# Optimization experiments

Measured on AMD Instinct MI355X. Metric: run time of the kernel, lower is better.

## Reference

```python
import jax, jax.numpy as jnp
import numpy as np

N = 50000
E = 800000
D_IN = 256
HID = 256
EPS = 1e-12


def _glorot(key, shape):
    fan_in, fan_out = shape[1], shape[0]
    lim = jnp.sqrt(6.0 / (fan_in + fan_out))
    return jax.random.uniform(key, shape, jnp.float32, -lim, lim)


def setup_inputs() -> dict:
    key = jax.random.key(0)
    ks = jax.random.split(key, 8)
    x = jax.random.normal(ks[0], (N, D_IN), jnp.float32)
    edge_index = jax.random.randint(ks[1], (2, E), 0, N, jnp.int64)
    # SAGEConv params: lin_l (neighbor, with bias), lin_r (root, no bias)
    W1l = _glorot(ks[2], (HID, D_IN))
    b1l = jnp.zeros((HID,), jnp.float32)
    W1r = _glorot(ks[3], (HID, D_IN))
    W2l = _glorot(ks[4], (HID, HID))
    b2l = jnp.zeros((HID,), jnp.float32)
    W2r = _glorot(ks[5], (HID, HID))
    return {"x": x, "edge_index": edge_index,
            "W1l": W1l, "b1l": b1l, "W1r": W1r,
            "W2l": W2l, "b2l": b2l, "W2r": W2r}


def _sage_conv(x, src, dst, Wl, bl, Wr, num_nodes):
    # mean aggregation of source features onto destination nodes
    agg = jax.ops.segment_sum(x[src], dst, num_segments=num_nodes)          # [N, d]
    cnt = jax.ops.segment_sum(jnp.ones((src.shape[0],), x.dtype), dst,
                              num_segments=num_nodes)                        # [N]
    mean = agg / jnp.maximum(cnt, 1.0)[:, None]
    out = mean @ Wl.T + bl + x @ Wr.T                                        # [N, out]
    # L2 normalize (normalize=True)
    norm = jnp.linalg.norm(out, axis=-1, keepdims=True)
    return out / jnp.maximum(norm, EPS)


def reference(x, edge_index, W1l, b1l, W1r, W2l, b2l, W2r):
    src, dst = edge_index[0], edge_index[1]
    n = x.shape[0]
    h = _sage_conv(x, src, dst, W1l, b1l, W1r, n)
    h = jax.nn.relu(h)
    h = _sage_conv(h, src, dst, W2l, b2l, W2r, n)
    return h
```

## Files before the change

kernel.cpp:

```cpp
#include <hip/hip_runtime.h>
#include <hip/hip_bf16.h>


#define DD 256
#define NPB 128

typedef unsigned short ushort_t;
using bf16x8 = __attribute__((ext_vector_type(8))) short;
using f32x4  = __attribute__((ext_vector_type(4))) float;

static __device__ __forceinline__ float b2f(ushort_t u) {
    __hip_bfloat16 h = *reinterpret_cast<__hip_bfloat16*>(&u);
    return __bfloat162float(h);
}
static __device__ __forceinline__ ushort_t f2b(float f) {
    __hip_bfloat16 h = __float2bfloat16(f);
    return *reinterpret_cast<ushort_t*>(&h);
}

static __device__ __forceinline__ void load16(const ushort_t* g, ushort_t* l) {
    __builtin_amdgcn_global_load_lds(
        (const __attribute__((address_space(1))) unsigned*)(g),
        (__attribute__((address_space(3))) unsigned*)(l),
        16, 0, 0);
}


__global__ __launch_bounds__(256) void prep_kernel(
        const int* __restrict__ ei, int* __restrict__ cnt, int E, int eb,
        const float* __restrict__ x, ushort_t* __restrict__ abuf, int xe, int cxb,
        const float* __restrict__ w1l, const float* __restrict__ w1r,
        const float* __restrict__ w2l, const float* __restrict__ w2r,
        ushort_t* __restrict__ wc1, ushort_t* __restrict__ wc2) {
    int b = blockIdx.x;
    if (b < eb) {
        int e = b * 256 + threadIdx.x;
        if (e < E) atomicAdd(&cnt[ei[E + e]], 1);
        return;
    }
    b -= eb;
    if (b < cxb) {
        int i = (b * 256 + threadIdx.x) * 8;
        if (i + 8 > xe) return;
        int row = i >> 8, col = i & 255;
        float4 a = *(const float4*)(x + i);
        float4 c = *(const float4*)(x + i + 4);
        ushort_t o[8] = {f2b(a.x), f2b(a.y), f2b(a.z), f2b(a.w),
                         f2b(c.x), f2b(c.y), f2b(c.z), f2b(c.w)};
        *(int4*)(abuf + (size_t)row * 512 + 256 + col) = *(const int4*)o;
        return;
    }
    b -= cxb;
    {
        int i = (b * 256 + threadIdx.x) * 8;
        int which = i >> 16;
        int o = i & 65535;
        int row = o >> 8, col = o & 255;
        const float* src = (which == 0) ? w1l : (which == 1) ? w1r
                          : (which == 2) ? w2l : w2r;
        ushort_t* dst = ((which < 2) ? wc1 : wc2)
                        + (size_t)row * 512 + (which & 1) * 256 + col;
        float4 a = *(const float4*)(src + o);
        float4 c = *(const float4*)(src + o + 4);
        ushort_t ov[8] = {f2b(a.x), f2b(a.y), f2b(a.z), f2b(a.w),
                          f2b(c.x), f2b(c.y), f2b(c.z), f2b(c.w)};
        *(int4*)dst = *(const int4*)ov;
    }
}


__global__ __launch_bounds__(256) void scan_partial_kernel(const int* __restrict__ cnt,
                                                           int* __restrict__ part, int n) {
    __shared__ int ws[4];
    int tid = threadIdx.x;
    int wave = tid >> 6, lane = tid & 63;
    int i0 = blockIdx.x * 2048 + tid * 8;
    int sum = 0;
    if (i0 + 8 <= n) {
        int4 a = *(const int4*)(cnt + i0);
        int4 b = *(const int4*)(cnt + i0 + 4);
        sum = a.x + a.y + a.z + a.w + b.x + b.y + b.z + b.w;
    } else {
        for (int j = i0; j < n; j++) sum += cnt[j];
    }
    #pragma unroll
    for (int off = 1; off < 64; off <<= 1) sum += __shfl_xor(sum, off);
    if (lane == 0) ws[wave] = sum;
    __syncthreads();
    if (tid == 0) part[blockIdx.x] = ws[0] + ws[1] + ws[2] + ws[3];
}

__global__ __launch_bounds__(256) void scan_final_kernel(const int* __restrict__ cnt,
                                                         const int* __restrict__ part,
                                                         int* __restrict__ offs,
                                                         int* __restrict__ bcur,
                                                         int n, int E, int nb) {
    __shared__ int wt[4];
    __shared__ int sbase;
    int tid = threadIdx.x;
    int wave = tid >> 6, lane = tid & 63;
    if (tid < 64) {
        int pv = (tid < nb) ? part[tid] : 0;
        int incl = pv;
        #pragma unroll
        for (int off = 1; off < 64; off <<= 1) {
            int t = __shfl_up(incl, off);
            if (tid >= off) incl += t;
        }
        if (tid == (int)blockIdx.x) sbase = incl - pv;
    }
    int i0 = blockIdx.x * 2048 + tid * 8;
    int v[8], s[8];
    int run = 0;
    if (i0 + 8 <= n) {
        int4 a = *(const int4*)(cnt + i0);
        int4 b = *(const int4*)(cnt + i0 + 4);
        v[0] = a.x; v[1] = a.y; v[2] = a.z; v[3] = a.w;
        v[4] = b.x; v[5] = b.y; v[6] = b.z; v[7] = b.w;
    } else {
        #pragma unroll
        for (int j = 0; j < 8; j++) v[j] = (i0 + j < n) ? cnt[i0 + j] : 0;
    }
    #pragma unroll
    for (int j = 0; j < 8; j++) { run += v[j]; s[j] = run; }
    int tsum = run;
    int incl = tsum;
    #pragma unroll
    for (int off = 1; off < 64; off <<= 1) {
        int t = __shfl_up(incl, off);
        if (lane >= off) incl += t;
    }
    if (lane == 63) wt[wave] = incl;
    __syncthreads();
    int woff = 0;
    for (int w = 0; w < wave; w++) woff += wt[w];
    int texcl = sbase + woff + (incl - tsum);
    #pragma unroll
    for (int j = 0; j < 8; j++) {
        int idx = i0 + j;
        if (idx < n) {
            int e = texcl + s[j] - v[j];
            offs[idx] = e;
            if ((idx & (NPB - 1)) == 0) bcur[idx / NPB] = e;
        }
    }
    if (blockIdx.x == 0 && tid == 0) offs[n] = E;
}


__global__ __launch_bounds__(256) void part_kernel(const int* __restrict__ ei,
                                                   int* __restrict__ bcur,
                                                   int2* __restrict__ stage,
                                                   int E, int nbuck) {
    __shared__ int hist[512];
    __shared__ int gbase[512];
    int tid = threadIdx.x;
    for (int i = tid; i < nbuck; i += 256) hist[i] = 0;
    __syncthreads();
    int sv[8], dv[8], bk[8], rk[8];
    #pragma unroll
    for (int j = 0; j < 8; j++) {
        int e = blockIdx.x * 2048 + j * 256 + tid;
        if (e < E) {
            sv[j] = ei[e];
            dv[j] = ei[E + e];
            bk[j] = dv[j] / NPB;
            rk[j] = atomicAdd(&hist[bk[j]], 1);
        } else bk[j] = -1;
    }
    __syncthreads();
    for (int i = tid; i < nbuck; i += 256) {
        int h = hist[i];
        gbase[i] = h ? atomicAdd(&bcur[i], h) : 0;
    }
    __syncthreads();
    #pragma unroll
    for (int j = 0; j < 8; j++)
        if (bk[j] >= 0) {
            int p = gbase[bk[j]] + rk[j];
            stage[p] = make_int2(sv[j], dv[j]);
        }
}

__global__ __launch_bounds__(256) void group_kernel(const int2* __restrict__ stage,
                                                    const int* __restrict__ offs,
                                                    int* __restrict__ csr, int N) {
    __shared__ int lcur[NPB];
    int b = blockIdx.x;
    int lo = b * NPB;
    int hi = min(N, lo + NPB);
    int tid = threadIdx.x;
    if (tid < hi - lo) lcur[tid] = offs[lo + tid];
    __syncthreads();
    int base = offs[lo];
    int m = offs[hi] - base;
    for (int t = tid; t < m; t += 256) {
        int2 v = stage[base + t];
        int p = atomicAdd(&lcur[v.y - lo], 1);
        csr[p] = v.x;
    }
}


static __device__ __forceinline__ void add8(float* acc, int4 v) {
    const unsigned* u = (const unsigned*)&v;
    #pragma unroll
    for (int j = 0; j < 4; j++) {
        acc[2 * j]     += __uint_as_float(u[j] << 16);
        acc[2 * j + 1] += __uint_as_float(u[j] & 0xffff0000u);
    }
}

__global__ __launch_bounds__(256) void agg_kernel(const ushort_t* __restrict__ X,
                                                  const int* __restrict__ csr,
                                                  const int* __restrict__ offs,
                                                  ushort_t* __restrict__ mean, int N) {
    int wv = threadIdx.x >> 6;
    int lane = threadIdx.x & 63;
    int half = lane >> 5;
    int c = lane & 31;
    int node = blockIdx.x * 4 + wv;
    if (node >= N) return;
    int beg = offs[node], end = offs[node + 1];

    float acc[8];
    #pragma unroll
    for (int j = 0; j < 8; j++) acc[j] = 0.f;

    const ushort_t* base = X + (size_t)c * 8;
    int i = beg;
    for (; i + 8 <= end; i += 8) {
        int s0 = csr[i + half];
        int s1 = csr[i + 2 + half];
        int s2 = csr[i + 4 + half];
        int s3 = csr[i + 6 + half];
        int4 v0 = *(const int4*)(base + (size_t)s0 * 512);
        int4 v1 = *(const int4*)(base + (size_t)s1 * 512);
        int4 v2 = *(const int4*)(base + (size_t)s2 * 512);
        int4 v3 = *(const int4*)(base + (size_t)s3 * 512);
        add8(acc, v0); add8(acc, v1); add8(acc, v2); add8(acc, v3);
    }
    for (; i + 2 <= end; i += 2) {
        int s0 = csr[i + half];
        int4 v0 = *(const int4*)(base + (size_t)s0 * 512);
        add8(acc, v0);
    }
    if (i < end && half == 0) {
        int s0 = csr[i];
        int4 v0 = *(const int4*)(base + (size_t)s0 * 512);
        add8(acc, v0);
    }

    #pragma unroll
    for (int j = 0; j < 8; j++) acc[j] += __shfl_xor(acc[j], 32);

    if (half == 0) {
        float scale = 1.f / fmaxf((float)(end - beg), 1.f);
        ushort_t o[8];
        #pragma unroll
        for (int j = 0; j < 8; j++) o[j] = f2b(acc[j] * scale);
        *(int4*)(mean + (size_t)node * 512 + c * 8) = *(const int4*)o;
    }
}


__global__ __launch_bounds__(512, 4) void gemm_norm_kernel(
        const ushort_t* __restrict__ abuf,
        const ushort_t* __restrict__ W,
        const float*    __restrict__ bias,
        ushort_t* __restrict__ outb,
        float*    __restrict__ outf,
        int ostride,
        int N, int relu) {
    __shared__ union {
        struct {
            ushort_t As[128 * 64];
            ushort_t Bs[256 * 64];
        } s;
        ushort_t ebuf[64 * 264];
    } u;
    __shared__ float rowsq[128];

    int tid = threadIdx.x;
    int wave = tid >> 6, lane = tid & 63;
    int quad = lane >> 4, m16 = lane & 15;
    int swz = m16 & 7;
    int rowhalf = wave >> 2;
    int colq = wave & 3;
    int rowbase = blockIdx.x * 128;

    if (tid < 128) rowsq[tid] = 0.f;

    f32x4 acc[4][4];
    #pragma unroll
    for (int i = 0; i < 4; i++)
        #pragma unroll
        for (int j = 0; j < 4; j++)
            acc[i][j] = (f32x4){0.f, 0.f, 0.f, 0.f};

    const ushort_t* Ag = abuf + (size_t)rowbase * 512;

    for (int ki = 0; ki < 8; ki++) {
        int kb = ki * 64;
        __syncthreads();
        #pragma unroll
        for (int t = 0; t < 2; t++) {
            int instr = wave * 2 + t;
            int flat = instr * 64 + lane;
            int row = flat >> 3, cc = flat & 7;
            int ccg = cc ^ (row & 7);
            load16(Ag + (size_t)row * 512 + kb + ccg * 8, &u.s.As[instr * 512]);
        }
        #pragma unroll
        for (int t = 0; t < 4; t++) {
            int instr = wave * 4 + t;
            int flat = instr * 64 + lane;
            int row = flat >> 3, cc = flat & 7;
            int ccg = cc ^ (row & 7);
            load16(W + (size_t)row * 512 + kb + ccg * 8, &u.s.Bs[instr * 512]);
        }
        __syncthreads();

        #pragma unroll
        for (int ks = 0; ks < 2; ks++) {
            int cbase = ks * 4 + quad;
            bf16x8 af[4], bfr[4];
            #pragma unroll
            for (int rt = 0; rt < 4; rt++) {
                int r = rowhalf * 64 + rt * 16 + m16;
                af[rt] = *(const bf16x8*)&u.s.As[r * 64 + (cbase ^ swz) * 8];
            }
            #pragma unroll
            for (int ct = 0; ct < 4; ct++) {
                int r = colq * 64 + ct * 16 + m16;
                bfr[ct] = *(const bf16x8*)&u.s.Bs[r * 64 + (cbase ^ swz) * 8];
            }
            #pragma unroll
            for (int rt = 0; rt < 4; rt++)
                #pragma unroll
                for (int ct = 0; ct < 4; ct++)
                    acc[rt][ct] = __builtin_amdgcn_mfma_f32_16x16x32_bf16(
                        af[rt], bfr[ct], acc[rt][ct], 0, 0, 0);
        }
    }

    float bvals[4];
    #pragma unroll
    for (int ct = 0; ct < 4; ct++)
        bvals[ct] = bias[colq * 64 + ct * 16 + m16];
    #pragma unroll
    for (int rt = 0; rt < 4; rt++) {
        #pragma unroll
        for (int reg = 0; reg < 4; reg++) {
            float s = 0.f;
            #pragma unroll
            for (int ct = 0; ct < 4; ct++) {
                float v = acc[rt][ct][reg] + bvals[ct];
                acc[rt][ct][reg] = v;
                s += v * v;
            }
            #pragma unroll
            for (int off = 1; off < 16; off <<= 1)
                s += __shfl_xor(s, off);
            if (m16 == 0)
                atomicAdd(&rowsq[rowhalf * 64 + rt * 16 + quad * 4 + reg], s);
        }
    }
    __syncthreads();

    #pragma unroll
    for (int p = 0; p < 2; p++) {
        if (rowhalf == p) {
            #pragma unroll
            for (int rt = 0; rt < 4; rt++) {
                #pragma unroll
                for (int reg = 0; reg < 4; reg++) {
                    int rl = rt * 16 + quad * 4 + reg;
                    float inv = 1.f / fmaxf(sqrtf(rowsq[p * 64 + rl]), 1e-12f);
                    #pragma unroll
                    for (int ct = 0; ct < 4; ct++) {
                        float v = acc[rt][ct][reg] * inv;
                        if (relu) v = fmaxf(v, 0.f);
                        int col = colq * 64 + ct * 16 + m16;
                        u.ebuf[rl * 264 + col] = f2b(v);
                    }
                }
            }
        }
        __syncthreads();
        #pragma unroll
        for (int j = 0; j < 4; j++) {
            int flat = j * 512 + tid;
            int row = flat >> 5, cc = flat & 31;
            int gr = rowbase + p * 64 + row;
            if (gr < N) {
                bf16x8 v = *(const bf16x8*)&u.ebuf[row * 264 + cc * 8];
                if (outf) {
                    float4 f0, f1;
                    f0.x = b2f((ushort_t)v[0]); f0.y = b2f((ushort_t)v[1]);
                    f0.z = b2f((ushort_t)v[2]); f0.w = b2f((ushort_t)v[3]);
                    f1.x = b2f((ushort_t)v[4]); f1.y = b2f((ushort_t)v[5]);
                    f1.z = b2f((ushort_t)v[6]); f1.w = b2f((ushort_t)v[7]);
                    float* ptr = outf + (size_t)gr * ostride + cc * 8;
                    *(float4*)ptr = f0;
                    *(float4*)(ptr + 4) = f1;
                } else {
                    *(bf16x8*)(outb + (size_t)gr * ostride + cc * 8) = v;
                }
            }
        }
        __syncthreads();
    }
}


static inline size_t align_up(size_t x, size_t a) { return (x + a - 1) & ~(a - 1); }

extern "C" void kernel_launch(void* const* d_in, const int* in_sizes, int n_in,
                              void* d_out, int out_size, void* d_ws, size_t ws_size,
                              hipStream_t stream) {
    const float* x   = (const float*)d_in[0];
    const int*   ei  = (const int*)d_in[1];
    const float* W1l = (const float*)d_in[2];
    const float* b1l = (const float*)d_in[3];
    const float* W1r = (const float*)d_in[4];
    const float* W2l = (const float*)d_in[5];
    const float* b2l = (const float*)d_in[6];
    const float* W2r = (const float*)d_in[7];

    int N = in_sizes[0] / DD;
    int E = in_sizes[1] / 2;
    int nbuck = (N + NPB - 1) / NPB;

    char* ws = (char*)d_ws;
    size_t off = 0;
    int* cnt = (int*)(ws + off);      off = align_up(off + (size_t)N * 4, 256);
    int* offs = (int*)(ws + off);     off = align_up(off + (size_t)(N + 1) * 4, 256);
    int* bcur = (int*)(ws + off);     off = align_up(off + (size_t)512 * 4, 256);
    int* part = (int*)(ws + off);     off = align_up(off + (size_t)64 * 4, 256);
    int* csr = (int*)(ws + off);      off = align_up(off + (size_t)E * 4, 256);
    int2* stage = (int2*)(ws + off);  off = align_up(off + (size_t)E * 8, 256);
    ushort_t* abuf = (ushort_t*)(ws + off);  off = align_up(off + (size_t)N * 512 * 2, 256);
    ushort_t* wc1 = (ushort_t*)(ws + off);   off = align_up(off + (size_t)256 * 512 * 2, 256);
    ushort_t* wc2 = (ushort_t*)(ws + off);   off = align_up(off + (size_t)256 * 512 * 2, 256);

    hipMemsetAsync(cnt, 0, (size_t)N * 4, stream);

    int xe = N * DD;
    int eb = (E + 255) / 256;
    int cxb = (xe / 8 + 255) / 256;
    int cwb = (4 * DD * DD / 8) / 256;
    prep_kernel<<<eb + cxb + cwb, 256, 0, stream>>>(ei, cnt, E, eb,
                                                    x, abuf, xe, cxb,
                                                    W1l, W1r, W2l, W2r, wc1, wc2);

    int nb = (N + 2047) / 2048;
    scan_partial_kernel<<<nb, 256, 0, stream>>>(cnt, part, N);
    scan_final_kernel<<<nb, 256, 0, stream>>>(cnt, part, offs, bcur, N, E, nb);

    int pb = (E + 2047) / 2048;
    part_kernel<<<pb, 256, 0, stream>>>(ei, bcur, stage, E, nbuck);
    group_kernel<<<nbuck, 256, 0, stream>>>(stage, offs, csr, N);

    int gb = (N + 127) / 128;
    int ab = (N + 3) / 4;

    agg_kernel<<<ab, 256, 0, stream>>>(abuf + 256, csr, offs, abuf, N);
    gemm_norm_kernel<<<gb, 512, 0, stream>>>(abuf, wc1, b1l,
                                             abuf + 256, (float*)nullptr, 512, N, 1);

    agg_kernel<<<ab, 256, 0, stream>>>(abuf + 256, csr, offs, abuf, N);
    gemm_norm_kernel<<<gb, 512, 0, stream>>>(abuf, wc2, b2l,
                                             (ushort_t*)nullptr, (float*)d_out, DD, N, 0);
}
```

Baseline: 331.8 us.

## Fuse neighbor mean aggregation into the GEMM+normalize kernel via shared memory

Each layer now gathers and averages neighbor features for a 64-row tile straight into shared memory, then runs the MFMA GEMM against that tile plus the root features, instead of writing mean features to global memory and reading them back in a separate kernel. Features move from an interleaved 512-wide buffer to separate 256-wide x and h buffers, so the layer output no longer overwrites its own input. The tile shrinks from 128 to 64 rows. This costs a larger LDS footprint (about 32KB extra for the mean tile) and possibly lower occupancy, and the gather phase can no longer overlap with GEMM work from other kernels.

```diff
diff --git a/kernel.cpp b/kernel.cpp
--- a/kernel.cpp
+++ b/kernel.cpp
@@ -28,7 +28,7 @@
 
 __global__ __launch_bounds__(256) void prep_kernel(
         const int* __restrict__ ei, int* __restrict__ cnt, int E, int eb,
-        const float* __restrict__ x, ushort_t* __restrict__ abuf, int xe, int cxb,
+        const float* __restrict__ x, ushort_t* __restrict__ xb, int xe, int cxb,
         const float* __restrict__ w1l, const float* __restrict__ w1r,
         const float* __restrict__ w2l, const float* __restrict__ w2r,
         ushort_t* __restrict__ wc1, ushort_t* __restrict__ wc2) {
@@ -42,12 +42,11 @@
     if (b < cxb) {
         int i = (b * 256 + threadIdx.x) * 8;
         if (i + 8 > xe) return;
-        int row = i >> 8, col = i & 255;
         float4 a = *(const float4*)(x + i);
         float4 c = *(const float4*)(x + i + 4);
         ushort_t o[8] = {f2b(a.x), f2b(a.y), f2b(a.z), f2b(a.w),
                          f2b(c.x), f2b(c.y), f2b(c.z), f2b(c.w)};
-        *(int4*)(abuf + (size_t)row * 512 + 256 + col) = *(const int4*)o;
+        *(int4*)(xb + i) = *(const int4*)o;
         return;
     }
     b -= cxb;
@@ -211,106 +210,93 @@
     }
 }
 
-__global__ __launch_bounds__(256) void agg_kernel(const ushort_t* __restrict__ X,
-                                                  const int* __restrict__ csr,
-                                                  const int* __restrict__ offs,
-                                                  ushort_t* __restrict__ mean, int N) {
-    int wv = threadIdx.x >> 6;
-    int lane = threadIdx.x & 63;
-    int half = lane >> 5;
-    int c = lane & 31;
-    int node = blockIdx.x * 4 + wv;
-    if (node >= N) return;
-    int beg = offs[node], end = offs[node + 1];
-
-    float acc[8];
-    #pragma unroll
-    for (int j = 0; j < 8; j++) acc[j] = 0.f;
-
-    const ushort_t* base = X + (size_t)c * 8;
-    int i = beg;
-    for (; i + 8 <= end; i += 8) {
-        int s0 = csr[i + half];
-        int s1 = csr[i + 2 + half];
-        int s2 = csr[i + 4 + half];
-        int s3 = csr[i + 6 + half];
-        int4 v0 = *(const int4*)(base + (size_t)s0 * 512);
-        int4 v1 = *(const int4*)(base + (size_t)s1 * 512);
-        int4 v2 = *(const int4*)(base + (size_t)s2 * 512);
-        int4 v3 = *(const int4*)(base + (size_t)s3 * 512);
-        add8(acc, v0); add8(acc, v1); add8(acc, v2); add8(acc, v3);
-    }
-    for (; i + 2 <= end; i += 2) {
-        int s0 = csr[i + half];
-        int4 v0 = *(const int4*)(base + (size_t)s0 * 512);
-        add8(acc, v0);
-    }
-    if (i < end && half == 0) {
-        int s0 = csr[i];
-        int4 v0 = *(const int4*)(base + (size_t)s0 * 512);
-        add8(acc, v0);
-    }
-
-    #pragma unroll
-    for (int j = 0; j < 8; j++) acc[j] += __shfl_xor(acc[j], 32);
-
-    if (half == 0) {
-        float scale = 1.f / fmaxf((float)(end - beg), 1.f);
-        ushort_t o[8];
-        #pragma unroll
-        for (int j = 0; j < 8; j++) o[j] = f2b(acc[j] * scale);
-        *(int4*)(mean + (size_t)node * 512 + c * 8) = *(const int4*)o;
-    }
-}
-
-
-__global__ __launch_bounds__(512, 4) void gemm_norm_kernel(
-        const ushort_t* __restrict__ abuf,
+__global__ __launch_bounds__(512, 4) void sage_layer_kernel(
+        const ushort_t* __restrict__ F,
+        const int* __restrict__ csr,
+        const int* __restrict__ offs,
         const ushort_t* __restrict__ W,
         const float*    __restrict__ bias,
         ushort_t* __restrict__ outb,
         float*    __restrict__ outf,
-        int ostride,
         int N, int relu) {
     __shared__ union {
         struct {
-            ushort_t As[128 * 64];
+            ushort_t mean[64 * 256];
+            ushort_t As[64 * 64];
             ushort_t Bs[256 * 64];
         } s;
         ushort_t ebuf[64 * 264];
     } u;
-    __shared__ float rowsq[128];
+    __shared__ float rowsq[64];
 
     int tid = threadIdx.x;
     int wave = tid >> 6, lane = tid & 63;
+    int rowbase = blockIdx.x * 64;
+
+    if (tid < 64) rowsq[tid] = 0.f;
+
+    {
+        int half = lane >> 5;
+        int c = lane & 31;
+        const ushort_t* base = F + (size_t)c * 8;
+        for (int n = wave; n < 64; n += 8) {
+            int node = rowbase + n;
+            if (node >= N) break;
+            int beg = offs[node], end = offs[node + 1];
+            float acc[8];
+            #pragma unroll
+            for (int j = 0; j < 8; j++) acc[j] = 0.f;
+            int i = beg;
+            for (; i + 8 <= end; i += 8) {
+                int s0 = csr[i + half];
+                int s1 = csr[i + 2 + half];
+                int s2 = csr[i + 4 + half];
+                int s3 = csr[i + 6 + half];
+                int4 v0 = *(const int4*)(base + (size_t)s0 * 256);
+                int4 v1 = *(const int4*)(base + (size_t)s1 * 256);
+                int4 v2 = *(const int4*)(base + (size_t)s2 * 256);
+                int4 v3 = *(const int4*)(base + (size_t)s3 * 256);
+                add8(acc, v0); add8(acc, v1); add8(acc, v2); add8(acc, v3);
+            }
+            for (; i + 2 <= end; i += 2) {
+                int s0 = csr[i + half];
+                int4 v0 = *(const int4*)(base + (size_t)s0 * 256);
+                add8(acc, v0);
+            }
+            if (i < end && half == 0) {
+                int s0 = csr[i];
+                int4 v0 = *(const int4*)(base + (size_t)s0 * 256);
+                add8(acc, v0);
+            }
+            #pragma unroll
+            for (int j = 0; j < 8; j++) acc[j] += __shfl_xor(acc[j], 32);
+            if (half == 0) {
+                float scale = 1.f / fmaxf((float)(end - beg), 1.f);
+                ushort_t o[8];
+                #pragma unroll
+                for (int j = 0; j < 8; j++) o[j] = f2b(acc[j] * scale);
+                int phys = (c & 24) + ((c & 7) ^ (n & 7));
+                *(int4*)&u.s.mean[n * 256 + phys * 8] = *(const int4*)o;
+            }
+        }
+    }
+
     int quad = lane >> 4, m16 = lane & 15;
     int swz = m16 & 7;
-    int rowhalf = wave >> 2;
+    int wr = wave >> 2;
     int colq = wave & 3;
-    int rowbase = blockIdx.x * 128;
-
-    if (tid < 128) rowsq[tid] = 0.f;
-
-    f32x4 acc[4][4];
-    #pragma unroll
-    for (int i = 0; i < 4; i++)
+    const ushort_t* Ag = F + (size_t)rowbase * 256;
+
+    f32x4 acc[2][4];
+    #pragma unroll
+    for (int i = 0; i < 2; i++)
         #pragma unroll
         for (int j = 0; j < 4; j++)
             acc[i][j] = (f32x4){0.f, 0.f, 0.f, 0.f};
 
-    const ushort_t* Ag = abuf + (size_t)rowbase * 512;
-
-    for (int ki = 0; ki < 8; ki++) {
+    for (int ki = 0; ki < 4; ki++) {
         int kb = ki * 64;
         __syncthreads();
-        #pragma unroll
-        for (int t = 0; t < 2; t++) {
-            int instr = wave * 2 + t;
-            int flat = instr * 64 + lane;
-            int row = flat >> 3, cc = flat & 7;
-            int ccg = cc ^ (row & 7);
-            load16(Ag + (size_t)row * 512 + kb + ccg * 8, &u.s.As[instr * 512]);
-        }
         #pragma unroll
         for (int t = 0; t < 4; t++) {
             int instr = wave * 4 + t;
@@ -320,23 +306,22 @@
             load16(W + (size_t)row * 512 + kb + ccg * 8, &u.s.Bs[instr * 512]);
         }
         __syncthreads();
-
         #pragma unroll
         for (int ks = 0; ks < 2; ks++) {
-            int cbase = ks * 4 + quad;
-            bf16x8 af[4], bfr[4];
-            #pragma unroll
-            for (int rt = 0; rt < 4; rt++) {
-                int r = rowhalf * 64 + rt * 16 + m16;
-                af[rt] = *(const bf16x8*)&u.s.As[r * 64 + (cbase ^ swz) * 8];
+            int pc = ((ks * 4 + quad) ^ swz) * 8;
+            bf16x8 af[2], bfr[4];
+            #pragma unroll
+            for (int rt = 0; rt < 2; rt++) {
+                int r = wr * 32 + rt * 16 + m16;
+                af[rt] = *(const bf16x8*)&u.s.mean[r * 256 + kb + pc];
             }
             #pragma unroll
             for (int ct = 0; ct < 4; ct++) {
                 int r = colq * 64 + ct * 16 + m16;
-                bfr[ct] = *(const bf16x8*)&u.s.Bs[r * 64 + (cbase ^ swz) * 8];
-            }
-            #pragma unroll
-            for (int rt = 0; rt < 4; rt++)
+                bfr[ct] = *(const bf16x8*)&u.s.Bs[r * 64 + pc];
+            }
+            #pragma unroll
+            for (int rt = 0; rt < 2; rt++)
                 #pragma unroll
                 for (int ct = 0; ct < 4; ct++)
                     acc[rt][ct] = __builtin_amdgcn_mfma_f32_16x16x32_bf16(
@@ -344,12 +329,52 @@
         }
     }
 
+    for (int ki = 4; ki < 8; ki++) {
+        int kb = ki * 64;
+        __syncthreads();
+        #pragma unroll
+        for (int t = 0; t < 4; t++) {
+            int instr = wave * 4 + t;
+            int flat = instr * 64 + lane;
+            int row = flat >> 3, cc = flat & 7;
+            int ccg = cc ^ (row & 7);
+            load16(W + (size_t)row * 512 + kb + ccg * 8, &u.s.Bs[instr * 512]);
+        }
+        {
+            int row = tid >> 3, cc = tid & 7;
+            int ccg = cc ^ (row & 7);
+            load16(Ag + (size_t)row * 256 + (kb - 256) + ccg * 8, &u.s.As[wave * 512]);
+        }
+        __syncthreads();
+        #pragma unroll
+        for (int ks = 0; ks < 2; ks++) {
+            int pc = ((ks * 4 + quad) ^ swz) * 8;
+            bf16x8 af[2], bfr[4];
+            #pragma unroll
+            for (int rt = 0; rt < 2; rt++) {
+                int r = wr * 32 + rt * 16 + m16;
+                af[rt] = *(const bf16x8*)&u.s.As[r * 64 + pc];
+            }
+            #pragma unroll
+            for (int ct = 0; ct < 4; ct++) {
+                int r = colq * 64 + ct * 16 + m16;
+                bfr[ct] = *(const bf16x8*)&u.s.Bs[r * 64 + pc];
+            }
+            #pragma unroll
+            for (int rt = 0; rt < 2; rt++)
+                #pragma unroll
+                for (int ct = 0; ct < 4; ct++)
+                    acc[rt][ct] = __builtin_amdgcn_mfma_f32_16x16x32_bf16(
+                        af[rt], bfr[ct], acc[rt][ct], 0, 0, 0);
+        }
+    }
+
     float bvals[4];
     #pragma unroll
     for (int ct = 0; ct < 4; ct++)
         bvals[ct] = bias[colq * 64 + ct * 16 + m16];
     #pragma unroll
-    for (int rt = 0; rt < 4; rt++) {
+    for (int rt = 0; rt < 2; rt++) {
         #pragma unroll
         for (int reg = 0; reg < 4; reg++) {
             float s = 0.f;
@@ -363,53 +388,47 @@
             for (int off = 1; off < 16; off <<= 1)
                 s += __shfl_xor(s, off);
             if (m16 == 0)
-                atomicAdd(&rowsq[rowhalf * 64 + rt * 16 + quad * 4 + reg], s);
-        }
-    }
-    __syncthreads();
-
-    #pragma unroll
-    for (int p = 0; p < 2; p++) {
-        if (rowhalf == p) {
-            #pragma unroll
-            for (int rt = 0; rt < 4; rt++) {
-                #pragma unroll
-                for (int reg = 0; reg < 4; reg++) {
-                    int rl = rt * 16 + quad * 4 + reg;
-                    float inv = 1.f / fmaxf(sqrtf(rowsq[p * 64 + rl]), 1e-12f);
-                    #pragma unroll
-                    for (int ct = 0; ct < 4; ct++) {
-                        float v = acc[rt][ct][reg] * inv;
-                        if (relu) v = fmaxf(v, 0.f);
-                        int col = colq * 64 + ct * 16 + m16;
-                        u.ebuf[rl * 264 + col] = f2b(v);
-                    }
-                }
-            }
-        }
-        __syncthreads();
-        #pragma unroll
-        for (int j = 0; j < 4; j++) {
-            int flat = j * 512 + tid;
-            int row = flat >> 5, cc = flat & 31;
-            int gr = rowbase + p * 64 + row;
-            if (gr < N) {
-                bf16x8 v = *(const bf16x8*)&u.ebuf[row * 264 + cc * 8];
-                if (outf) {
-                    float4 f0, f1;
-                    f0.x = b2f((ushort_t)v[0]); f0.y = b2f((ushort_t)v[1]);
-                    f0.z = b2f((ushort_t)v[2]); f0.w = b2f((ushort_t)v[3]);
-                    f1.x = b2f((ushort_t)v[4]); f1.y = b2f((ushort_t)v[5]);
-                    f1.z = b2f((ushort_t)v[6]); f1.w = b2f((ushort_t)v[7]);
-                    float* ptr = outf + (size_t)gr * ostride + cc * 8;
-                    *(float4*)ptr = f0;
-                    *(float4*)(ptr + 4) = f1;
-                } else {
-                    *(bf16x8*)(outb + (size_t)gr * ostride + cc * 8) = v;
-                }
-            }
-        }
-        __syncthreads();
+                atomicAdd(&rowsq[wr * 32 + rt * 16 + quad * 4 + reg], s);
+        }
+    }
+    __syncthreads();
+
+    #pragma unroll
+    for (int rt = 0; rt < 2; rt++) {
+        #pragma unroll
+        for (int reg = 0; reg < 4; reg++) {
+            int rl = wr * 32 + rt * 16 + quad * 4 + reg;
+            float inv = 1.f / fmaxf(sqrtf(rowsq[rl]), 1e-12f);
+            #pragma unroll
+            for (int ct = 0; ct < 4; ct++) {
+                float v = acc[rt][ct][reg] * inv;
+                if (relu) v = fmaxf(v, 0.f);
+                int col = colq * 64 + ct * 16 + m16;
+                u.ebuf[rl * 264 + col] = f2b(v);
+            }
+        }
+    }
+    __syncthreads();
+    #pragma unroll
+    for (int j = 0; j < 4; j++) {
+        int flat = j * 512 + tid;
+        int row = flat >> 5, cc = flat & 31;
+        int gr = rowbase + row;
+        if (gr < N) {
+            bf16x8 v = *(const bf16x8*)&u.ebuf[row * 264 + cc * 8];
+            if (outf) {
+                float4 f0, f1;
+                f0.x = b2f((ushort_t)v[0]); f0.y = b2f((ushort_t)v[1]);
+                f0.z = b2f((ushort_t)v[2]); f0.w = b2f((ushort_t)v[3]);
+                f1.x = b2f((ushort_t)v[4]); f1.y = b2f((ushort_t)v[5]);
+                f1.z = b2f((ushort_t)v[6]); f1.w = b2f((ushort_t)v[7]);
+                float* ptr = outf + (size_t)gr * 256 + cc * 8;
+                *(float4*)ptr = f0;
+                *(float4*)(ptr + 4) = f1;
+            } else {
+                *(bf16x8*)(outb + (size_t)gr * 256 + cc * 8) = v;
+            }
+        }
     }
 }
 
@@ -440,9 +459,10 @@
     int* part = (int*)(ws + off);     off = align_up(off + (size_t)64 * 4, 256);
     int* csr = (int*)(ws + off);      off = align_up(off + (size_t)E * 4, 256);
     int2* stage = (int2*)(ws + off);  off = align_up(off + (size_t)E * 8, 256);
-    ushort_t* abuf = (ushort_t*)(ws + off);  off = align_up(off + (size_t)N * 512 * 2, 256);
-    ushort_t* wc1 = (ushort_t*)(ws + off);   off = align_up(off + (size_t)256 * 512 * 2, 256);
-    ushort_t* wc2 = (ushort_t*)(ws + off);   off = align_up(off + (size_t)256 * 512 * 2, 256);
+    ushort_t* xb = (ushort_t*)(ws + off);  off = align_up(off + (size_t)(N + 64) * 256 * 2, 256);
+    ushort_t* hb = (ushort_t*)(ws + off);  off = align_up(off + (size_t)(N + 64) * 256 * 2, 256);
+    ushort_t* wc1 = (ushort_t*)(ws + off); off = align_up(off + (size_t)256 * 512 * 2, 256);
+    ushort_t* wc2 = (ushort_t*)(ws + off); off = align_up(off + (size_t)256 * 512 * 2, 256);
 
     hipMemsetAsync(cnt, 0, (size_t)N * 4, stream);
 
@@ -451,7 +471,7 @@
     int cxb = (xe / 8 + 255) / 256;
     int cwb = (4 * DD * DD / 8) / 256;
     prep_kernel<<<eb + cxb + cwb, 256, 0, stream>>>(ei, cnt, E, eb,
-                                                    x, abuf, xe, cxb,
+                                                    x, xb, xe, cxb,
                                                     W1l, W1r, W2l, W2r, wc1, wc2);
 
     int nb = (N + 2047) / 2048;
@@ -462,14 +482,10 @@
     part_kernel<<<pb, 256, 0, stream>>>(ei, bcur, stage, E, nbuck);
     group_kernel<<<nbuck, 256, 0, stream>>>(stage, offs, csr, N);
 
-    int gb = (N + 127) / 128;
-    int ab = (N + 3) / 4;
-
-    agg_kernel<<<ab, 256, 0, stream>>>(abuf + 256, csr, offs, abuf, N);
-    gemm_norm_kernel<<<gb, 512, 0, stream>>>(abuf, wc1, b1l,
-                                             abuf + 256, (float*)nullptr, 512, N, 1);
-
-    agg_kernel<<<ab, 256, 0, stream>>>(abuf + 256, csr, offs, abuf, N);
-    gemm_norm_kernel<<<gb, 512, 0, stream>>>(abuf, wc2, b2l,
-                                             (ushort_t*)nullptr, (float*)d_out, DD, N, 0);
-}
+    int gb = (N + 63) / 64;
+
+    sage_layer_kernel<<<gb, 512, 0, stream>>>(xb, csr, offs, wc1, b1l,
+                                              hb, (float*)nullptr, N, 1);
+    sage_layer_kernel<<<gb, 512, 0, stream>>>(hb, csr, offs, wc2, b2l,
+                                              (ushort_t*)nullptr, (float*)d_out, N, 0);
+}
```

Result: slower. 352.2 us (+6.1%).

## Slice node features into 32-column planes for cache-local gather aggregation

Applied to the files above, without the earlier changes.

Stores bf16 node features and means in a column-sliced layout: eight planes of 32 columns, each holding every node. The aggregation kernel assigns each block one slice, so the gathered working set per slice (about 3.2 MB) can stay in cache. Within a node, 16 edges are gathered in parallel with 64-byte rows and combined by shuffle reduction. The GEMM now reads A tiles from two separate sliced buffers (mean and features), and the mean buffer reuses the stage buffer memory. This adds strided row addressing in the GEMM loads and spreads the work for each node across eight blocks.

```diff
diff --git a/kernel.cpp b/kernel.cpp
--- a/kernel.cpp
+++ b/kernel.cpp
@@ -8,6 +8,7 @@
 typedef unsigned short ushort_t;
 using bf16x8 = __attribute__((ext_vector_type(8))) short;
 using f32x4  = __attribute__((ext_vector_type(4))) float;
+using i32x4  = __attribute__((ext_vector_type(4))) int;
 
 static __device__ __forceinline__ float b2f(ushort_t u) {
     __hip_bfloat16 h = *reinterpret_cast<__hip_bfloat16*>(&u);
@@ -25,10 +26,15 @@
         16, 0, 0);
 }
 
+static __device__ __forceinline__ size_t sma(int npad, int node, int col) {
+    return ((size_t)(col >> 5) * npad + node) * 32 + (col & 31);
+}
+
 
 __global__ __launch_bounds__(256) void prep_kernel(
         const int* __restrict__ ei, int* __restrict__ cnt, int E, int eb,
-        const float* __restrict__ x, ushort_t* __restrict__ abuf, int xe, int cxb,
+        const float* __restrict__ x, ushort_t* __restrict__ xb, int xe, int cxb,
+        int npad,
         const float* __restrict__ w1l, const float* __restrict__ w1r,
         const float* __restrict__ w2l, const float* __restrict__ w2r,
         ushort_t* __restrict__ wc1, ushort_t* __restrict__ wc2) {
@@ -42,12 +48,12 @@
     if (b < cxb) {
         int i = (b * 256 + threadIdx.x) * 8;
         if (i + 8 > xe) return;
-        int row = i >> 8, col = i & 255;
+        int node = i >> 8, col = i & 255;
         float4 a = *(const float4*)(x + i);
         float4 c = *(const float4*)(x + i + 4);
         ushort_t o[8] = {f2b(a.x), f2b(a.y), f2b(a.z), f2b(a.w),
                          f2b(c.x), f2b(c.y), f2b(c.z), f2b(c.w)};
-        *(int4*)(abuf + (size_t)row * 512 + 256 + col) = *(const int4*)o;
+        *(i32x4*)(xb + sma(npad, node, col)) = *(const i32x4*)o;
         return;
     }
     b -= cxb;
@@ -64,7 +70,7 @@
         float4 c = *(const float4*)(src + o + 4);
         ushort_t ov[8] = {f2b(a.x), f2b(a.y), f2b(a.z), f2b(a.w),
                           f2b(c.x), f2b(c.y), f2b(c.z), f2b(c.w)};
-        *(int4*)dst = *(const int4*)ov;
+        *(i32x4*)dst = *(const i32x4*)ov;
     }
 }
 
@@ -202,7 +208,7 @@
 }
 
 
-static __device__ __forceinline__ void add8(float* acc, int4 v) {
+static __device__ __forceinline__ void add8(float* acc, i32x4 v) {
     const unsigned* u = (const unsigned*)&v;
     #pragma unroll
     for (int j = 0; j < 4; j++) {
@@ -211,67 +217,54 @@
     }
 }
 
-__global__ __launch_bounds__(256) void agg_kernel(const ushort_t* __restrict__ X,
+__global__ __launch_bounds__(256) void agg_kernel(const ushort_t* __restrict__ F,
                                                   const int* __restrict__ csr,
                                                   const int* __restrict__ offs,
-                                                  ushort_t* __restrict__ mean, int N) {
-    int wv = threadIdx.x >> 6;
-    int lane = threadIdx.x & 63;
-    int half = lane >> 5;
-    int c = lane & 31;
-    int node = blockIdx.x * 4 + wv;
-    if (node >= N) return;
-    int beg = offs[node], end = offs[node + 1];
-
-    float acc[8];
-    #pragma unroll
-    for (int j = 0; j < 8; j++) acc[j] = 0.f;
-
-    const ushort_t* base = X + (size_t)c * 8;
-    int i = beg;
-    for (; i + 8 <= end; i += 8) {
-        int s0 = csr[i + half];
-        int s1 = csr[i + 2 + half];
-        int s2 = csr[i + 4 + half];
-        int s3 = csr[i + 6 + half];
-        int4 v0 = *(const int4*)(base + (size_t)s0 * 512);
-        int4 v1 = *(const int4*)(base + (size_t)s1 * 512);
-        int4 v2 = *(const int4*)(base + (size_t)s2 * 512);
-        int4 v3 = *(const int4*)(base + (size_t)s3 * 512);
-        add8(acc, v0); add8(acc, v1); add8(acc, v2); add8(acc, v3);
-    }
-    for (; i + 2 <= end; i += 2) {
-        int s0 = csr[i + half];
-        int4 v0 = *(const int4*)(base + (size_t)s0 * 512);
-        add8(acc, v0);
-    }
-    if (i < end && half == 0) {
-        int s0 = csr[i];
-        int4 v0 = *(const int4*)(base + (size_t)s0 * 512);
-        add8(acc, v0);
-    }
-
-    #pragma unroll
-    for (int j = 0; j < 8; j++) acc[j] += __shfl_xor(acc[j], 32);
-
-    if (half == 0) {
-        float scale = 1.f / fmaxf((float)(end - beg), 1.f);
-        ushort_t o[8];
-        #pragma unroll
-        for (int j = 0; j < 8; j++) o[j] = f2b(acc[j] * scale);
-        *(int4*)(mean + (size_t)node * 512 + c * 8) = *(const int4*)o;
+                                                  ushort_t* __restrict__ mean,
+                                                  int N, int npad) {
+    int s = blockIdx.x & 7;
+    int g0 = (blockIdx.x >> 3) * 64;
+    int wv = threadIdx.x >> 6, lane = threadIdx.x & 63;
+    int nb = lane >> 2;
+    int ch = lane & 3;
+    const ushort_t* Fs = F + (size_t)s * npad * 32 + ch * 8;
+    ushort_t* Ms = mean + (size_t)s * npad * 32 + ch * 8;
+    int nend = min(N, g0 + 64);
+    for (int n = g0 + wv; n < nend; n += 4) {
+        int beg = offs[n], end = offs[n + 1];
+        float acc[8];
+        #pragma unroll
+        for (int j = 0; j < 8; j++) acc[j] = 0.f;
+        for (int i = beg + nb; i < end; i += 16) {
+            int src = __builtin_nontemporal_load(csr + i);
+            i32x4 v = *(const i32x4*)(Fs + (size_t)src * 32);
+            add8(acc, v);
+        }
+        #pragma unroll
+        for (int off = 4; off < 64; off <<= 1) {
+            #pragma unroll
+            for (int j = 0; j < 8; j++) acc[j] += __shfl_xor(acc[j], off);
+        }
+        if (nb == 0) {
+            float scale = 1.f / fmaxf((float)(end - beg), 1.f);
+            ushort_t o[8];
+            #pragma unroll
+            for (int j = 0; j < 8; j++) o[j] = f2b(acc[j] * scale);
+            __builtin_nontemporal_store(*(const i32x4*)o,
+                                        (i32x4*)(Ms + (size_t)n * 32));
+        }
     }
 }
 
 
 __global__ __launch_bounds__(512, 4) void gemm_norm_kernel(
-        const ushort_t* __restrict__ abuf,
+        const ushort_t* __restrict__ meanb,
+        const ushort_t* __restrict__ fb,
         const ushort_t* __restrict__ W,
         const float*    __restrict__ bias,
         ushort_t* __restrict__ outb,
         float*    __restrict__ outf,
-        int ostride,
-        int N, int relu) {
+        int npad, int N, int relu) {
     __shared__ union {
         struct {
             ushort_t As[128 * 64];
@@ -298,10 +291,10 @@
         for (int j = 0; j < 4; j++)
             acc[i][j] = (f32x4){0.f, 0.f, 0.f, 0.f};
 
-    const ushort_t* Ag = abuf + (size_t)rowbase * 512;
-
     for (int ki = 0; ki < 8; ki++) {
         int kb = ki * 64;
+        const ushort_t* Ab = (ki < 4) ? meanb : fb;
+        int kl = kb & 255;
         __syncthreads();
         #pragma unroll
         for (int t = 0; t < 2; t++) {
@@ -309,7 +302,8 @@
             int flat = instr * 64 + lane;
             int row = flat >> 3, cc = flat & 7;
             int ccg = cc ^ (row & 7);
-            load16(Ag + (size_t)row * 512 + kb + ccg * 8, &u.s.As[instr * 512]);
+            int c = kl + ccg * 8;
+            load16(Ab + sma(npad, rowbase + row, c), &u.s.As[instr * 512]);
         }
         #pragma unroll
         for (int t = 0; t < 4; t++) {
@@ -328,12 +322,12 @@
             #pragma unroll
             for (int rt = 0; rt < 4; rt++) {
                 int r = rowhalf * 64 + rt * 16 + m16;
-                af[rt] = *(const bf16x8*)&u.s.As[r * 64 + (cbase ^ swz) * 8];
+                af[rt] = *(const bf16x8*)&u.s.As[r * 64 + ((cbase ^ swz)) * 8];
             }
             #pragma unroll
             for (int ct = 0; ct < 4; ct++) {
                 int r = colq * 64 + ct * 16 + m16;
-                bfr[ct] = *(const bf16x8*)&u.s.Bs[r * 64 + (cbase ^ swz) * 8];
+                bfr[ct] = *(const bf16x8*)&u.s.Bs[r * 64 + ((cbase ^ swz)) * 8];
             }
             #pragma unroll
             for (int rt = 0; rt < 4; rt++)
@@ -401,11 +395,11 @@
                     f0.z = b2f((ushort_t)v[2]); f0.w = b2f((ushort_t)v[3]);
                     f1.x = b2f((ushort_t)v[4]); f1.y = b2f((ushort_t)v[5]);
                     f1.z = b2f((ushort_t)v[6]); f1.w = b2f((ushort_t)v[7]);
-                    float* ptr = outf + (size_t)gr * ostride + cc * 8;
+                    float* ptr = outf + (size_t)gr * 256 + cc * 8;
                     *(float4*)ptr = f0;
                     *(float4*)(ptr + 4) = f1;
                 } else {
-                    *(bf16x8*)(outb + (size_t)gr * ostride + cc * 8) = v;
+                    *(bf16x8*)(outb + sma(npad, gr, cc * 8)) = v;
                 }
             }
         }
@@ -430,6 +424,7 @@
 
     int N = in_sizes[0] / DD;
     int E = in_sizes[1] / 2;
+    int npad = N + 128;
     int nbuck = (N + NPB - 1) / NPB;
 
     char* ws = (char*)d_ws;
@@ -439,10 +434,15 @@
     int* bcur = (int*)(ws + off);     off = align_up(off + (size_t)512 * 4, 256);
     int* part = (int*)(ws + off);     off = align_up(off + (size_t)64 * 4, 256);
     int* csr = (int*)(ws + off);      off = align_up(off + (size_t)E * 4, 256);
-    int2* stage = (int2*)(ws + off);  off = align_up(off + (size_t)E * 8, 256);
-    ushort_t* abuf = (ushort_t*)(ws + off);  off = align_up(off + (size_t)N * 512 * 2, 256);
-    ushort_t* wc1 = (ushort_t*)(ws + off);   off = align_up(off + (size_t)256 * 512 * 2, 256);
-    ushort_t* wc2 = (ushort_t*)(ws + off);   off = align_up(off + (size_t)256 * 512 * 2, 256);
+    size_t sstage = off;
+    int2* stage = (int2*)(ws + sstage);
+    size_t meansz = (size_t)npad * 32 * 8 * 2;
+    off = align_up(sstage + ((size_t)E * 8 > meansz ? (size_t)E * 8 : meansz), 256);
+    ushort_t* meanb = (ushort_t*)(ws + sstage);
+    ushort_t* xb = (ushort_t*)(ws + off);  off = align_up(off + meansz, 256);
+    ushort_t* hb = (ushort_t*)(ws + off);  off = align_up(off + meansz, 256);
+    ushort_t* wc1 = (ushort_t*)(ws + off); off = align_up(off + (size_t)256 * 512 * 2, 256);
+    ushort_t* wc2 = (ushort_t*)(ws + off); off = align_up(off + (size_t)256 * 512 * 2, 256);
 
     hipMemsetAsync(cnt, 0, (size_t)N * 4, stream);
 
@@ -451,7 +451,7 @@
     int cxb = (xe / 8 + 255) / 256;
     int cwb = (4 * DD * DD / 8) / 256;
     prep_kernel<<<eb + cxb + cwb, 256, 0, stream>>>(ei, cnt, E, eb,
-                                                    x, abuf, xe, cxb,
+                                                    x, xb, xe, cxb, npad,
                                                     W1l, W1r, W2l, W2r, wc1, wc2);
 
     int nb = (N + 2047) / 2048;
@@ -462,14 +462,14 @@
     part_kernel<<<pb, 256, 0, stream>>>(ei, bcur, stage, E, nbuck);
     group_kernel<<<nbuck, 256, 0, stream>>>(stage, offs, csr, N);
 
+    int ab = 8 * ((N + 63) / 64);
     int gb = (N + 127) / 128;
-    int ab = (N + 3) / 4;
-
-    agg_kernel<<<ab, 256, 0, stream>>>(abuf + 256, csr, offs, abuf, N);
-    gemm_norm_kernel<<<gb, 512, 0, stream>>>(abuf, wc1, b1l,
-                                             abuf + 256, (float*)nullptr, 512, N, 1);
-
-    agg_kernel<<<ab, 256, 0, stream>>>(abuf + 256, csr, offs, abuf, N);
-    gemm_norm_kernel<<<gb, 512, 0, stream>>>(abuf, wc2, b2l,
-                                             (ushort_t*)nullptr, (float*)d_out, DD, N, 0);
-}
+
+    agg_kernel<<<ab, 256, 0, stream>>>(xb, csr, offs, meanb, N, npad);
+    gemm_norm_kernel<<<gb, 512, 0, stream>>>(meanb, xb, wc1, b1l,
+                                             hb, (float*)nullptr, npad, N, 1);
+
+    agg_kernel<<<ab, 256, 0, stream>>>(hb, csr, offs, meanb, N, npad);
+    gemm_norm_kernel<<<gb, 512, 0, stream>>>(meanb, hb, wc2, b2l,
+                                             (ushort_t*)nullptr, (float*)d_out, npad, N, 0);
+}
```

Result: slower. 532.8 us (+60.6%).
